# Optimization experiments

Hardware: AMD Instinct MI355X
Metric: run time of the kernel (lower is better)

The kernel has to match this reference:

```python
import jax, jax.numpy as jnp
import numpy as np

EMBED_DIM = 512
NUM_HEADS = 8
HEAD_DIM = EMBED_DIM // NUM_HEADS
B, T, S = 4, 2048, 2048
NEG_INF = jnp.float32(-1e30)


def setup_inputs() -> dict:
    key = jax.random.key(0)
    ks = jax.random.split(key, 12)
    std = 1.0 / np.sqrt(EMBED_DIM)
    d = {
        "query": jax.random.normal(ks[0], (B, T, EMBED_DIM), jnp.float32),
        "key": jax.random.normal(ks[1], (B, S, EMBED_DIM), jnp.float32),
        "value": jax.random.normal(ks[2], (B, S, EMBED_DIM), jnp.float32),
        "key_padding_mask": jnp.zeros((B, S), dtype=bool),
        "attn_mask": jnp.zeros((T, S), dtype=bool),
        "Wq": jax.random.normal(ks[3], (EMBED_DIM, EMBED_DIM), jnp.float32) * std,
        "bq": jnp.zeros((EMBED_DIM,), jnp.float32),
        "Wk": jax.random.normal(ks[4], (EMBED_DIM, EMBED_DIM), jnp.float32) * std,
        "bk": jnp.zeros((EMBED_DIM,), jnp.float32),
        "Wv": jax.random.normal(ks[5], (EMBED_DIM, EMBED_DIM), jnp.float32) * std,
        "bv": jnp.zeros((EMBED_DIM,), jnp.float32),
        "Wo": jax.random.normal(ks[6], (EMBED_DIM, EMBED_DIM), jnp.float32) * std,
        "bo": jnp.zeros((EMBED_DIM,), jnp.float32),
    }
    return d


def reference(query, key, value, key_padding_mask, attn_mask,
              Wq, bq, Wk, bk, Wv, bv, Wo, bo):
    scaling = HEAD_DIM ** (-0.5)
    # projections; Wx stored as [in, out] equivalent of torch Linear weight^T
    q = (query @ Wq + bq) * scaling            # [B, T, E]
    k = key @ Wk + bk                          # [B, S, E]
    v = value @ Wv + bv                        # [B, S, E]
    # split heads -> [B, H, T, Dh]
    q = q.reshape(B, T, NUM_HEADS, HEAD_DIM).transpose(0, 2, 1, 3)
    k = k.reshape(B, S, NUM_HEADS, HEAD_DIM).transpose(0, 2, 1, 3)
    v = v.reshape(B, S, NUM_HEADS, HEAD_DIM).transpose(0, 2, 1, 3)
    scores = jnp.einsum('bhtd,bhsd->bhts', q, k)  # [B, H, T, S]
    scores = jnp.where(attn_mask[None, None, :, :], NEG_INF, scores)
    scores = jnp.where(key_padding_mask[:, None, None, :], NEG_INF, scores)
    attn_weights = jax.nn.softmax(scores, axis=-1)
    # dropout=0 (eval/deterministic): attn_probs == attn_weights
    attn = jnp.einsum('bhts,bhsd->bhtd', attn_weights, v)
    attn = attn.transpose(0, 2, 1, 3).reshape(B, T, EMBED_DIM)
    output = attn @ Wo + bo
    return output, attn_weights
```

## Files before the change

### kernel.cpp

```cpp
#include <hip/hip_runtime.h>
#include <stdint.h>

#define BB 4
#define TT 2048
#define SS 2048
#define EE 512
#define HH 8
#define DH 64
#define NEG_INF_F (-1e30f)

__global__ __launch_bounds__(256) void proj_gemm(const float* __restrict__ A,
        const float* __restrict__ W, const float* __restrict__ bias,
        float* __restrict__ C, float alpha) {
    const int K = EE, N = EE;
    __shared__ float As[16][128 + 4];
    __shared__ float Bs[16][64 + 4];
    const int tid = threadIdx.x;
    const int tx = tid & 15;
    const int ty = tid >> 4;
    const int bm = blockIdx.y * 128;
    const int bn = blockIdx.x * 64;
    float acc[8][4] = {};
    for (int k0 = 0; k0 < K; k0 += 16) {
        #pragma unroll
        for (int j = 0; j < 2; ++j) {
            int f = tid + 256 * j;
            int row = f >> 2;
            int c4 = f & 3;
            float4 v = *reinterpret_cast<const float4*>(
                &A[(size_t)(bm + row) * K + k0 + c4 * 4]);
            As[c4 * 4 + 0][row] = v.x;
            As[c4 * 4 + 1][row] = v.y;
            As[c4 * 4 + 2][row] = v.z;
            As[c4 * 4 + 3][row] = v.w;
        }
        {
            int row = tid >> 4;
            int c4 = tid & 15;
            float4 v = *reinterpret_cast<const float4*>(
                &W[(size_t)(k0 + row) * N + bn + c4 * 4]);
            *reinterpret_cast<float4*>(&Bs[row][c4 * 4]) = v;
        }
        __syncthreads();
        #pragma unroll
        for (int kk = 0; kk < 16; ++kk) {
            float a[8], b[4];
            #pragma unroll
            for (int i = 0; i < 8; ++i) a[i] = As[kk][ty * 8 + i];
            #pragma unroll
            for (int j = 0; j < 4; ++j) b[j] = Bs[kk][tx * 4 + j];
            #pragma unroll
            for (int i = 0; i < 8; ++i)
                #pragma unroll
                for (int j = 0; j < 4; ++j)
                    acc[i][j] = fmaf(a[i], b[j], acc[i][j]);
        }
        __syncthreads();
    }
    #pragma unroll
    for (int i = 0; i < 8; ++i) {
        float4 o;
        o.x = (acc[i][0] + bias[bn + tx * 4 + 0]) * alpha;
        o.y = (acc[i][1] + bias[bn + tx * 4 + 1]) * alpha;
        o.z = (acc[i][2] + bias[bn + tx * 4 + 2]) * alpha;
        o.w = (acc[i][3] + bias[bn + tx * 4 + 3]) * alpha;
        *reinterpret_cast<float4*>(
            &C[(size_t)(bm + ty * 8 + i) * N + bn + tx * 4]) = o;
    }
}

__global__ __launch_bounds__(256) void scores_kernel(const float* __restrict__ q,
        const float* __restrict__ k, const uint8_t* __restrict__ am,
        const uint8_t* __restrict__ kpm, float* __restrict__ Sc) {
    const int bh = blockIdx.z;
    const int b = bh >> 3, h = bh & 7;
    const int t0 = blockIdx.y * 64;
    const int s0 = blockIdx.x * 64;
    __shared__ float Qs[DH][64 + 4];
    __shared__ float Ks[DH][64 + 4];
    const int tid = threadIdx.x;
    #pragma unroll
    for (int j = 0; j < 4; ++j) {
        int f = tid + 256 * j;
        int row = f >> 4;
        int c4 = f & 15;
        float4 vq = *reinterpret_cast<const float4*>(
            &q[(size_t)(b * TT + t0 + row) * EE + h * DH + c4 * 4]);
        Qs[c4 * 4 + 0][row] = vq.x; Qs[c4 * 4 + 1][row] = vq.y;
        Qs[c4 * 4 + 2][row] = vq.z; Qs[c4 * 4 + 3][row] = vq.w;
        float4 vk = *reinterpret_cast<const float4*>(
            &k[(size_t)(b * SS + s0 + row) * EE + h * DH + c4 * 4]);
        Ks[c4 * 4 + 0][row] = vk.x; Ks[c4 * 4 + 1][row] = vk.y;
        Ks[c4 * 4 + 2][row] = vk.z; Ks[c4 * 4 + 3][row] = vk.w;
    }
    __syncthreads();
    const int tx = tid & 15, ty = tid >> 4;
    float acc[4][4] = {};
    #pragma unroll 8
    for (int d = 0; d < DH; ++d) {
        float a[4], bv[4];
        #pragma unroll
        for (int i = 0; i < 4; ++i) a[i] = Qs[d][ty * 4 + i];
        #pragma unroll
        for (int j = 0; j < 4; ++j) bv[j] = Ks[d][tx * 4 + j];
        #pragma unroll
        for (int i = 0; i < 4; ++i)
            #pragma unroll
            for (int j = 0; j < 4; ++j)
                acc[i][j] = fmaf(a[i], bv[j], acc[i][j]);
    }
    uchar4 kv = *reinterpret_cast<const uchar4*>(&kpm[b * SS + s0 + tx * 4]);
    #pragma unroll
    for (int i = 0; i < 4; ++i) {
        int t = t0 + ty * 4 + i;
        uchar4 amv = *reinterpret_cast<const uchar4*>(
            &am[(size_t)t * SS + s0 + tx * 4]);
        float4 o;
        o.x = (amv.x | kv.x) ? NEG_INF_F : acc[i][0];
        o.y = (amv.y | kv.y) ? NEG_INF_F : acc[i][1];
        o.z = (amv.z | kv.z) ? NEG_INF_F : acc[i][2];
        o.w = (amv.w | kv.w) ? NEG_INF_F : acc[i][3];
        *reinterpret_cast<float4*>(
            &Sc[((size_t)bh * TT + t) * SS + s0 + tx * 4]) = o;
    }
}

__device__ __forceinline__ float wred_max(float v) {
    #pragma unroll
    for (int off = 32; off > 0; off >>= 1) v = fmaxf(v, __shfl_xor(v, off));
    return v;
}
__device__ __forceinline__ float wred_sum(float v) {
    #pragma unroll
    for (int off = 32; off > 0; off >>= 1) v += __shfl_xor(v, off);
    return v;
}

__global__ __launch_bounds__(256) void softmax_kernel(float* __restrict__ P) {
    const size_t base = (size_t)blockIdx.x * SS;
    const int tid = threadIdx.x;
    float4 x0 = *reinterpret_cast<const float4*>(&P[base + (size_t)tid * 4]);
    float4 x1 = *reinterpret_cast<const float4*>(&P[base + (size_t)(tid + 256) * 4]);
    float m = fmaxf(fmaxf(fmaxf(x0.x, x0.y), fmaxf(x0.z, x0.w)),
                    fmaxf(fmaxf(x1.x, x1.y), fmaxf(x1.z, x1.w)));
    m = wred_max(m);
    __shared__ float rmax[4];
    __shared__ float rsum[4];
    const int wid = tid >> 6, lane = tid & 63;
    if (lane == 0) rmax[wid] = m;
    __syncthreads();
    m = fmaxf(fmaxf(rmax[0], rmax[1]), fmaxf(rmax[2], rmax[3]));
    x0.x = __expf(x0.x - m); x0.y = __expf(x0.y - m);
    x0.z = __expf(x0.z - m); x0.w = __expf(x0.w - m);
    x1.x = __expf(x1.x - m); x1.y = __expf(x1.y - m);
    x1.z = __expf(x1.z - m); x1.w = __expf(x1.w - m);
    float s = x0.x + x0.y + x0.z + x0.w + x1.x + x1.y + x1.z + x1.w;
    s = wred_sum(s);
    if (lane == 0) rsum[wid] = s;
    __syncthreads();
    s = rsum[0] + rsum[1] + rsum[2] + rsum[3];
    const float inv = 1.0f / s;
    x0.x *= inv; x0.y *= inv; x0.z *= inv; x0.w *= inv;
    x1.x *= inv; x1.y *= inv; x1.z *= inv; x1.w *= inv;
    *reinterpret_cast<float4*>(&P[base + (size_t)tid * 4]) = x0;
    *reinterpret_cast<float4*>(&P[base + (size_t)(tid + 256) * 4]) = x1;
}

__global__ __launch_bounds__(256) void pv_kernel(const float* __restrict__ P,
        const float* __restrict__ v, float* __restrict__ ctx) {
    const int bh = blockIdx.y;
    const int b = bh >> 3, h = bh & 7;
    const int t0 = blockIdx.x * 128;
    __shared__ float Ps[16][128 + 4];
    __shared__ float Vs[16][64 + 4];
    const int tid = threadIdx.x;
    const int tx = tid & 15, ty = tid >> 4;
    float acc[8][4] = {};
    for (int s0 = 0; s0 < SS; s0 += 16) {
        #pragma unroll
        for (int j = 0; j < 2; ++j) {
            int f = tid + 256 * j;
            int row = f >> 2;
            int c4 = f & 3;
            float4 pv = *reinterpret_cast<const float4*>(
                &P[((size_t)bh * TT + t0 + row) * SS + s0 + c4 * 4]);
            Ps[c4 * 4 + 0][row] = pv.x; Ps[c4 * 4 + 1][row] = pv.y;
            Ps[c4 * 4 + 2][row] = pv.z; Ps[c4 * 4 + 3][row] = pv.w;
        }
        {
            int row = tid >> 4, c4 = tid & 15;
            float4 vv = *reinterpret_cast<const float4*>(
                &v[(size_t)(b * SS + s0 + row) * EE + h * DH + c4 * 4]);
            *reinterpret_cast<float4*>(&Vs[row][c4 * 4]) = vv;
        }
        __syncthreads();
        #pragma unroll
        for (int kk = 0; kk < 16; ++kk) {
            float a[8], bv[4];
            #pragma unroll
            for (int i = 0; i < 8; ++i) a[i] = Ps[kk][ty * 8 + i];
            #pragma unroll
            for (int j = 0; j < 4; ++j) bv[j] = Vs[kk][tx * 4 + j];
            #pragma unroll
            for (int i = 0; i < 8; ++i)
                #pragma unroll
                for (int j = 0; j < 4; ++j)
                    acc[i][j] = fmaf(a[i], bv[j], acc[i][j]);
        }
        __syncthreads();
    }
    #pragma unroll
    for (int i = 0; i < 8; ++i) {
        float4 o = make_float4(acc[i][0], acc[i][1], acc[i][2], acc[i][3]);
        *reinterpret_cast<float4*>(
            &ctx[(size_t)(b * TT + t0 + ty * 8 + i) * EE + h * DH + tx * 4]) = o;
    }
}

extern "C" void kernel_launch(void* const* d_in, const int* in_sizes, int n_in,
                              void* d_out, int out_size, void* d_ws, size_t ws_size,
                              hipStream_t stream) {
    const float*   query = (const float*)d_in[0];
    const float*   key   = (const float*)d_in[1];
    const float*   value = (const float*)d_in[2];
    const uint8_t* kpm   = (const uint8_t*)d_in[3];
    const uint8_t* am    = (const uint8_t*)d_in[4];
    const float* Wq = (const float*)d_in[5];  const float* bq = (const float*)d_in[6];
    const float* Wk = (const float*)d_in[7];  const float* bk = (const float*)d_in[8];
    const float* Wv = (const float*)d_in[9];  const float* bv = (const float*)d_in[10];
    const float* Wo = (const float*)d_in[11]; const float* bo = (const float*)d_in[12];

    float* out   = (float*)d_out;
    const size_t BTE = (size_t)BB * TT * EE;
    float* attnW = out + BTE;
    float* ws  = (float*)d_ws;
    float* qp  = ws;
    float* kp  = ws + BTE;
    float* vp  = ws + 2 * BTE;
    float* ctx = qp;

    const float scaling = 0.125f;
    dim3 gProj(EE / 64, (BB * TT) / 128);

    proj_gemm<<<gProj, 256, 0, stream>>>(query, Wq, bq, qp, scaling);
    proj_gemm<<<gProj, 256, 0, stream>>>(key,   Wk, bk, kp, 1.0f);
    proj_gemm<<<gProj, 256, 0, stream>>>(value, Wv, bv, vp, 1.0f);

    scores_kernel<<<dim3(SS / 64, TT / 64, BB * HH), 256, 0, stream>>>(
        qp, kp, am, kpm, attnW);
    softmax_kernel<<<BB * HH * TT, 256, 0, stream>>>(attnW);
    pv_kernel<<<dim3(TT / 128, BB * HH), 256, 0, stream>>>(attnW, vp, ctx);

    proj_gemm<<<gProj, 256, 0, stream>>>(ctx, Wo, bo, out, 1.0f);
}
```

Before: 1.451 ms.

## Fuse scores and softmax with two-pass bf16 MFMA, MFMA PV with transposed V

Replaces the separate scores, softmax and PV kernels with a two-pass kernel. The first pass computes QK^T using bf16 MFMA and keeps running max and sum, and the second recomputes scores and writes normalized probabilities. This removes the full write-then-read-modify-write of the attention-weight matrix. PV now uses bf16 MFMA, with V written transposed by a dedicated projection kernel. The cost is recomputing QK^T, reduced precision from bf16 inputs, and scattered scalar stores of attention weights and mask bytes, which may be poorly coalesced.

Result: faster. 1.298 ms (-10.5%).

```diff
diff --git a/kernel.cpp b/kernel.cpp
--- a/kernel.cpp
+++ b/kernel.cpp
@@ -9,6 +9,37 @@
 #define DH 64
 #define NEG_INF_F (-1e30f)
 
+using short8 = __attribute__((ext_vector_type(8))) short;
+using f32x4  = __attribute__((ext_vector_type(4))) float;
+
+__device__ __forceinline__ unsigned short f2bf(float f) {
+    unsigned int u = __float_as_uint(f);
+    unsigned int r = (u + 0x7FFFu + ((u >> 16) & 1u)) >> 16;
+    return (unsigned short)r;
+}
+__device__ __forceinline__ unsigned int pack2(float a, float b) {
+    return (unsigned int)f2bf(a) | ((unsigned int)f2bf(b) << 16);
+}
+__device__ __forceinline__ short8 cvt_frag(float4 a, float4 b) {
+    short8 r;
+    r[0] = (short)f2bf(a.x); r[1] = (short)f2bf(a.y);
+    r[2] = (short)f2bf(a.z); r[3] = (short)f2bf(a.w);
+    r[4] = (short)f2bf(b.x); r[5] = (short)f2bf(b.y);
+    r[6] = (short)f2bf(b.z); r[7] = (short)f2bf(b.w);
+    return r;
+}
+
+__device__ __forceinline__ void stage_tile_bf16(const float* src_base, size_t row_stride,
+        unsigned short (*dst)[72], int tid) {
+    const int row = tid >> 2;
+    const int cg  = (tid & 3) * 16;
+    const float4* s4 = reinterpret_cast<const float4*>(src_base + (size_t)row * row_stride + cg);
+    float4 a = s4[0], b = s4[1], c = s4[2], d = s4[3];
+    uint4* d4 = reinterpret_cast<uint4*>(&dst[row][cg]);
+    d4[0] = make_uint4(pack2(a.x, a.y), pack2(a.z, a.w), pack2(b.x, b.y), pack2(b.z, b.w));
+    d4[1] = make_uint4(pack2(c.x, c.y), pack2(c.z, c.w), pack2(d.x, d.y), pack2(d.z, d.w));
+}
+
 __global__ __launch_bounds__(256) void proj_gemm(const float* __restrict__ A,
         const float* __restrict__ W, const float* __restrict__ bias,
         float* __restrict__ C, float alpha) {
@@ -16,29 +47,21 @@
     __shared__ float As[16][128 + 4];
     __shared__ float Bs[16][64 + 4];
     const int tid = threadIdx.x;
-    const int tx = tid & 15;
-    const int ty = tid >> 4;
-    const int bm = blockIdx.y * 128;
-    const int bn = blockIdx.x * 64;
+    const int tx = tid & 15, ty = tid >> 4;
+    const int bm = blockIdx.y * 128, bn = blockIdx.x * 64;
     float acc[8][4] = {};
     for (int k0 = 0; k0 < K; k0 += 16) {
         #pragma unroll
         for (int j = 0; j < 2; ++j) {
             int f = tid + 256 * j;
-            int row = f >> 2;
-            int c4 = f & 3;
-            float4 v = *reinterpret_cast<const float4*>(
-                &A[(size_t)(bm + row) * K + k0 + c4 * 4]);
-            As[c4 * 4 + 0][row] = v.x;
-            As[c4 * 4 + 1][row] = v.y;
-            As[c4 * 4 + 2][row] = v.z;
-            As[c4 * 4 + 3][row] = v.w;
+            int row = f >> 2, c4 = f & 3;
+            float4 v = *reinterpret_cast<const float4*>(&A[(size_t)(bm + row) * K + k0 + c4 * 4]);
+            As[c4 * 4 + 0][row] = v.x; As[c4 * 4 + 1][row] = v.y;
+            As[c4 * 4 + 2][row] = v.z; As[c4 * 4 + 3][row] = v.w;
         }
         {
-            int row = tid >> 4;
-            int c4 = tid & 15;
-            float4 v = *reinterpret_cast<const float4*>(
-                &W[(size_t)(k0 + row) * N + bn + c4 * 4]);
+            int row = tid >> 4, c4 = tid & 15;
+            float4 v = *reinterpret_cast<const float4*>(&W[(size_t)(k0 + row) * N + bn + c4 * 4]);
             *reinterpret_cast<float4*>(&Bs[row][c4 * 4]) = v;
         }
         __syncthreads();
@@ -64,157 +87,214 @@
         o.y = (acc[i][1] + bias[bn + tx * 4 + 1]) * alpha;
         o.z = (acc[i][2] + bias[bn + tx * 4 + 2]) * alpha;
         o.w = (acc[i][3] + bias[bn + tx * 4 + 3]) * alpha;
-        *reinterpret_cast<float4*>(
-            &C[(size_t)(bm + ty * 8 + i) * N + bn + tx * 4]) = o;
-    }
-}
-
-__global__ __launch_bounds__(256) void scores_kernel(const float* __restrict__ q,
-        const float* __restrict__ k, const uint8_t* __restrict__ am,
-        const uint8_t* __restrict__ kpm, float* __restrict__ Sc) {
-    const int bh = blockIdx.z;
-    const int b = bh >> 3, h = bh & 7;
-    const int t0 = blockIdx.y * 64;
-    const int s0 = blockIdx.x * 64;
-    __shared__ float Qs[DH][64 + 4];
-    __shared__ float Ks[DH][64 + 4];
-    const int tid = threadIdx.x;
-    #pragma unroll
-    for (int j = 0; j < 4; ++j) {
-        int f = tid + 256 * j;
-        int row = f >> 4;
-        int c4 = f & 15;
-        float4 vq = *reinterpret_cast<const float4*>(
-            &q[(size_t)(b * TT + t0 + row) * EE + h * DH + c4 * 4]);
-        Qs[c4 * 4 + 0][row] = vq.x; Qs[c4 * 4 + 1][row] = vq.y;
-        Qs[c4 * 4 + 2][row] = vq.z; Qs[c4 * 4 + 3][row] = vq.w;
-        float4 vk = *reinterpret_cast<const float4*>(
-            &k[(size_t)(b * SS + s0 + row) * EE + h * DH + c4 * 4]);
-        Ks[c4 * 4 + 0][row] = vk.x; Ks[c4 * 4 + 1][row] = vk.y;
-        Ks[c4 * 4 + 2][row] = vk.z; Ks[c4 * 4 + 3][row] = vk.w;
-    }
-    __syncthreads();
-    const int tx = tid & 15, ty = tid >> 4;
-    float acc[4][4] = {};
-    #pragma unroll 8
-    for (int d = 0; d < DH; ++d) {
-        float a[4], bv[4];
-        #pragma unroll
-        for (int i = 0; i < 4; ++i) a[i] = Qs[d][ty * 4 + i];
-        #pragma unroll
-        for (int j = 0; j < 4; ++j) bv[j] = Ks[d][tx * 4 + j];
-        #pragma unroll
-        for (int i = 0; i < 4; ++i)
-            #pragma unroll
-            for (int j = 0; j < 4; ++j)
-                acc[i][j] = fmaf(a[i], bv[j], acc[i][j]);
-    }
-    uchar4 kv = *reinterpret_cast<const uchar4*>(&kpm[b * SS + s0 + tx * 4]);
-    #pragma unroll
-    for (int i = 0; i < 4; ++i) {
-        int t = t0 + ty * 4 + i;
-        uchar4 amv = *reinterpret_cast<const uchar4*>(
-            &am[(size_t)t * SS + s0 + tx * 4]);
-        float4 o;
-        o.x = (amv.x | kv.x) ? NEG_INF_F : acc[i][0];
-        o.y = (amv.y | kv.y) ? NEG_INF_F : acc[i][1];
-        o.z = (amv.z | kv.z) ? NEG_INF_F : acc[i][2];
-        o.w = (amv.w | kv.w) ? NEG_INF_F : acc[i][3];
-        *reinterpret_cast<float4*>(
-            &Sc[((size_t)bh * TT + t) * SS + s0 + tx * 4]) = o;
-    }
-}
-
-__device__ __forceinline__ float wred_max(float v) {
-    #pragma unroll
-    for (int off = 32; off > 0; off >>= 1) v = fmaxf(v, __shfl_xor(v, off));
-    return v;
-}
-__device__ __forceinline__ float wred_sum(float v) {
-    #pragma unroll
-    for (int off = 32; off > 0; off >>= 1) v += __shfl_xor(v, off);
-    return v;
-}
-
-__global__ __launch_bounds__(256) void softmax_kernel(float* __restrict__ P) {
-    const size_t base = (size_t)blockIdx.x * SS;
-    const int tid = threadIdx.x;
-    float4 x0 = *reinterpret_cast<const float4*>(&P[base + (size_t)tid * 4]);
-    float4 x1 = *reinterpret_cast<const float4*>(&P[base + (size_t)(tid + 256) * 4]);
-    float m = fmaxf(fmaxf(fmaxf(x0.x, x0.y), fmaxf(x0.z, x0.w)),
-                    fmaxf(fmaxf(x1.x, x1.y), fmaxf(x1.z, x1.w)));
-    m = wred_max(m);
-    __shared__ float rmax[4];
-    __shared__ float rsum[4];
-    const int wid = tid >> 6, lane = tid & 63;
-    if (lane == 0) rmax[wid] = m;
-    __syncthreads();
-    m = fmaxf(fmaxf(rmax[0], rmax[1]), fmaxf(rmax[2], rmax[3]));
-    x0.x = __expf(x0.x - m); x0.y = __expf(x0.y - m);
-    x0.z = __expf(x0.z - m); x0.w = __expf(x0.w - m);
-    x1.x = __expf(x1.x - m); x1.y = __expf(x1.y - m);
-    x1.z = __expf(x1.z - m); x1.w = __expf(x1.w - m);
-    float s = x0.x + x0.y + x0.z + x0.w + x1.x + x1.y + x1.z + x1.w;
-    s = wred_sum(s);
-    if (lane == 0) rsum[wid] = s;
-    __syncthreads();
-    s = rsum[0] + rsum[1] + rsum[2] + rsum[3];
-    const float inv = 1.0f / s;
-    x0.x *= inv; x0.y *= inv; x0.z *= inv; x0.w *= inv;
-    x1.x *= inv; x1.y *= inv; x1.z *= inv; x1.w *= inv;
-    *reinterpret_cast<float4*>(&P[base + (size_t)tid * 4]) = x0;
-    *reinterpret_cast<float4*>(&P[base + (size_t)(tid + 256) * 4]) = x1;
-}
-
-__global__ __launch_bounds__(256) void pv_kernel(const float* __restrict__ P,
-        const float* __restrict__ v, float* __restrict__ ctx) {
-    const int bh = blockIdx.y;
-    const int b = bh >> 3, h = bh & 7;
-    const int t0 = blockIdx.x * 128;
-    __shared__ float Ps[16][128 + 4];
-    __shared__ float Vs[16][64 + 4];
+        *reinterpret_cast<float4*>(&C[(size_t)(bm + ty * 8 + i) * N + bn + tx * 4]) = o;
+    }
+}
+
+__global__ __launch_bounds__(256) void proj_gemm_vT(const float* __restrict__ A,
+        const float* __restrict__ W, const float* __restrict__ bias,
+        float* __restrict__ vpT) {
+    const int K = EE, N = EE;
+    __shared__ float As[16][128 + 4];
+    __shared__ float Bs[16][64 + 4];
     const int tid = threadIdx.x;
     const int tx = tid & 15, ty = tid >> 4;
+    const int bm = blockIdx.y * 128, bn = blockIdx.x * 64;
     float acc[8][4] = {};
-    for (int s0 = 0; s0 < SS; s0 += 16) {
+    for (int k0 = 0; k0 < K; k0 += 16) {
         #pragma unroll
         for (int j = 0; j < 2; ++j) {
             int f = tid + 256 * j;
-            int row = f >> 2;
-            int c4 = f & 3;
-            float4 pv = *reinterpret_cast<const float4*>(
-                &P[((size_t)bh * TT + t0 + row) * SS + s0 + c4 * 4]);
-            Ps[c4 * 4 + 0][row] = pv.x; Ps[c4 * 4 + 1][row] = pv.y;
-            Ps[c4 * 4 + 2][row] = pv.z; Ps[c4 * 4 + 3][row] = pv.w;
+            int row = f >> 2, c4 = f & 3;
+            float4 v = *reinterpret_cast<const float4*>(&A[(size_t)(bm + row) * K + k0 + c4 * 4]);
+            As[c4 * 4 + 0][row] = v.x; As[c4 * 4 + 1][row] = v.y;
+            As[c4 * 4 + 2][row] = v.z; As[c4 * 4 + 3][row] = v.w;
         }
         {
             int row = tid >> 4, c4 = tid & 15;
-            float4 vv = *reinterpret_cast<const float4*>(
-                &v[(size_t)(b * SS + s0 + row) * EE + h * DH + c4 * 4]);
-            *reinterpret_cast<float4*>(&Vs[row][c4 * 4]) = vv;
+            float4 v = *reinterpret_cast<const float4*>(&W[(size_t)(k0 + row) * N + bn + c4 * 4]);
+            *reinterpret_cast<float4*>(&Bs[row][c4 * 4]) = v;
         }
         __syncthreads();
         #pragma unroll
         for (int kk = 0; kk < 16; ++kk) {
-            float a[8], bv[4];
-            #pragma unroll
-            for (int i = 0; i < 8; ++i) a[i] = Ps[kk][ty * 8 + i];
-            #pragma unroll
-            for (int j = 0; j < 4; ++j) bv[j] = Vs[kk][tx * 4 + j];
+            float a[8], b[4];
+            #pragma unroll
+            for (int i = 0; i < 8; ++i) a[i] = As[kk][ty * 8 + i];
+            #pragma unroll
+            for (int j = 0; j < 4; ++j) b[j] = Bs[kk][tx * 4 + j];
             #pragma unroll
             for (int i = 0; i < 8; ++i)
                 #pragma unroll
                 for (int j = 0; j < 4; ++j)
-                    acc[i][j] = fmaf(a[i], bv[j], acc[i][j]);
-        }
-        __syncthreads();
-    }
-    #pragma unroll
-    for (int i = 0; i < 8; ++i) {
-        float4 o = make_float4(acc[i][0], acc[i][1], acc[i][2], acc[i][3]);
-        *reinterpret_cast<float4*>(
-            &ctx[(size_t)(b * TT + t0 + ty * 8 + i) * EE + h * DH + tx * 4]) = o;
-    }
+                    acc[i][j] = fmaf(a[i], b[j], acc[i][j]);
+        }
+        __syncthreads();
+    }
+    const int bb = bm >> 11;
+    const int sb = (bm & (SS - 1)) + ty * 8;
+    #pragma unroll
+    for (int j = 0; j < 4; ++j) {
+        const int n = bn + tx * 4 + j;
+        const float bvj = bias[n];
+        float4 o0 = make_float4(acc[0][j] + bvj, acc[1][j] + bvj, acc[2][j] + bvj, acc[3][j] + bvj);
+        float4 o1 = make_float4(acc[4][j] + bvj, acc[5][j] + bvj, acc[6][j] + bvj, acc[7][j] + bvj);
+        float* dst = &vpT[((size_t)bb * EE + n) * SS + sb];
+        *reinterpret_cast<float4*>(dst) = o0;
+        *reinterpret_cast<float4*>(dst + 4) = o1;
+    }
+}
+
+__global__ __launch_bounds__(256) void flash_scores(const float* __restrict__ qp,
+        const float* __restrict__ kp, const uint8_t* __restrict__ am,
+        const uint8_t* __restrict__ kpm, float* __restrict__ attnW) {
+    const int bh = blockIdx.y;
+    const int b = bh >> 3, h = bh & 7;
+    const int t0 = blockIdx.x * 64;
+    __shared__ unsigned short Ks[64][72];
+    const int tid = threadIdx.x;
+    const int lane = tid & 63, wid = tid >> 6;
+    const int lc = lane & 15, lg = lane >> 4;
+
+    short8 aq[2];
+    {
+        const float* qrow = &qp[(size_t)(b * TT + t0 + wid * 16 + lc) * EE + h * DH];
+        #pragma unroll
+        for (int kc = 0; kc < 2; ++kc) {
+            float4 f0 = *reinterpret_cast<const float4*>(qrow + kc * 32 + lg * 8);
+            float4 f1 = *reinterpret_cast<const float4*>(qrow + kc * 32 + lg * 8 + 4);
+            aq[kc] = cvt_frag(f0, f1);
+        }
+    }
+    const int trow = t0 + wid * 16 + lg * 4;
+    float mrun[4], lrun[4];
+    #pragma unroll
+    for (int r = 0; r < 4; ++r) { mrun[r] = -3.0e38f; lrun[r] = 0.0f; }
+
+    for (int st = 0; st < 32; ++st) {
+        const int s0 = st * 64;
+        stage_tile_bf16(&kp[(size_t)(b * SS + s0) * EE + h * DH], EE, Ks, tid);
+        __syncthreads();
+        float sv[4][4];
+        float tmax[4];
+        #pragma unroll
+        for (int r = 0; r < 4; ++r) tmax[r] = -3.0e38f;
+        #pragma unroll
+        for (int ct = 0; ct < 4; ++ct) {
+            const int brow = ct * 16 + lc;
+            short8 b0 = *reinterpret_cast<const short8*>(&Ks[brow][lg * 8]);
+            short8 b1 = *reinterpret_cast<const short8*>(&Ks[brow][32 + lg * 8]);
+            f32x4 c = {0.0f, 0.0f, 0.0f, 0.0f};
+            c = __builtin_amdgcn_mfma_f32_16x16x32_bf16(aq[0], b0, c, 0, 0, 0);
+            c = __builtin_amdgcn_mfma_f32_16x16x32_bf16(aq[1], b1, c, 0, 0, 0);
+            const int s = s0 + ct * 16 + lc;
+            const bool kpb = kpm[b * SS + s] != 0;
+            #pragma unroll
+            for (int r = 0; r < 4; ++r) {
+                const bool mk = kpb || (am[(size_t)(trow + r) * SS + s] != 0);
+                const float scv = mk ? NEG_INF_F : c[r];
+                sv[ct][r] = scv;
+                tmax[r] = fmaxf(tmax[r], scv);
+            }
+        }
+        __syncthreads();
+        #pragma unroll
+        for (int r = 0; r < 4; ++r) {
+            #pragma unroll
+            for (int mm = 8; mm >= 1; mm >>= 1)
+                tmax[r] = fmaxf(tmax[r], __shfl_xor(tmax[r], mm, 16));
+        }
+        float ts[4] = {0.0f, 0.0f, 0.0f, 0.0f};
+        #pragma unroll
+        for (int ct = 0; ct < 4; ++ct)
+            #pragma unroll
+            for (int r = 0; r < 4; ++r) {
+                const float mnew = fmaxf(mrun[r], tmax[r]);
+                ts[r] += __expf(sv[ct][r] - mnew);
+            }
+        #pragma unroll
+        for (int r = 0; r < 4; ++r) {
+            const float mnew = fmaxf(mrun[r], tmax[r]);
+            #pragma unroll
+            for (int mm = 8; mm >= 1; mm >>= 1)
+                ts[r] += __shfl_xor(ts[r], mm, 16);
+            lrun[r] = lrun[r] * __expf(mrun[r] - mnew) + ts[r];
+            mrun[r] = mnew;
+        }
+    }
+    float linv[4];
+    #pragma unroll
+    for (int r = 0; r < 4; ++r) linv[r] = 1.0f / lrun[r];
+
+    for (int st = 0; st < 32; ++st) {
+        const int s0 = st * 64;
+        stage_tile_bf16(&kp[(size_t)(b * SS + s0) * EE + h * DH], EE, Ks, tid);
+        __syncthreads();
+        #pragma unroll
+        for (int ct = 0; ct < 4; ++ct) {
+            const int brow = ct * 16 + lc;
+            short8 b0 = *reinterpret_cast<const short8*>(&Ks[brow][lg * 8]);
+            short8 b1 = *reinterpret_cast<const short8*>(&Ks[brow][32 + lg * 8]);
+            f32x4 c = {0.0f, 0.0f, 0.0f, 0.0f};
+            c = __builtin_amdgcn_mfma_f32_16x16x32_bf16(aq[0], b0, c, 0, 0, 0);
+            c = __builtin_amdgcn_mfma_f32_16x16x32_bf16(aq[1], b1, c, 0, 0, 0);
+            const int s = s0 + ct * 16 + lc;
+            const bool kpb = kpm[b * SS + s] != 0;
+            #pragma unroll
+            for (int r = 0; r < 4; ++r) {
+                const bool mk = kpb || (am[(size_t)(trow + r) * SS + s] != 0);
+                const float scv = mk ? NEG_INF_F : c[r];
+                const float p = __expf(scv - mrun[r]) * linv[r];
+                attnW[((size_t)bh * TT + trow + r) * SS + s] = p;
+            }
+        }
+        __syncthreads();
+    }
+}
+
+__global__ __launch_bounds__(256) void pv_mfma(const float* __restrict__ P,
+        const float* __restrict__ vpT, float* __restrict__ ctx) {
+    const int bh = blockIdx.y;
+    const int b = bh >> 3, h = bh & 7;
+    const int t0 = blockIdx.x * 64;
+    __shared__ unsigned short Vt[64][72];
+    const int tid = threadIdx.x;
+    const int lane = tid & 63, wid = tid >> 6;
+    const int lc = lane & 15, lg = lane >> 4;
+
+    f32x4 acc[4];
+    #pragma unroll
+    for (int ct = 0; ct < 4; ++ct) acc[ct] = (f32x4){0.0f, 0.0f, 0.0f, 0.0f};
+
+    const float* prow = &P[((size_t)bh * TT + t0 + wid * 16 + lc) * SS];
+
+    for (int st = 0; st < 32; ++st) {
+        const int s0 = st * 64;
+        stage_tile_bf16(&vpT[((size_t)b * EE + h * DH) * SS + s0], SS, Vt, tid);
+        __syncthreads();
+        short8 ap[2];
+        #pragma unroll
+        for (int kc = 0; kc < 2; ++kc) {
+            float4 f0 = *reinterpret_cast<const float4*>(prow + s0 + kc * 32 + lg * 8);
+            float4 f1 = *reinterpret_cast<const float4*>(prow + s0 + kc * 32 + lg * 8 + 4);
+            ap[kc] = cvt_frag(f0, f1);
+        }
+        #pragma unroll
+        for (int ct = 0; ct < 4; ++ct) {
+            const int brow = ct * 16 + lc;
+            short8 b0 = *reinterpret_cast<const short8*>(&Vt[brow][lg * 8]);
+            short8 b1 = *reinterpret_cast<const short8*>(&Vt[brow][32 + lg * 8]);
+            acc[ct] = __builtin_amdgcn_mfma_f32_16x16x32_bf16(ap[0], b0, acc[ct], 0, 0, 0);
+            acc[ct] = __builtin_amdgcn_mfma_f32_16x16x32_bf16(ap[1], b1, acc[ct], 0, 0, 0);
+        }
+        __syncthreads();
+    }
+    const int trow = t0 + wid * 16 + lg * 4;
+    #pragma unroll
+    for (int ct = 0; ct < 4; ++ct)
+        #pragma unroll
+        for (int r = 0; r < 4; ++r)
+            ctx[(size_t)(b * TT + trow + r) * EE + h * DH + ct * 16 + lc] = acc[ct][r];
 }
 
 extern "C" void kernel_launch(void* const* d_in, const int* in_sizes, int n_in,
@@ -236,20 +316,18 @@
     float* ws  = (float*)d_ws;
     float* qp  = ws;
     float* kp  = ws + BTE;
-    float* vp  = ws + 2 * BTE;
+    float* vpT = ws + 2 * BTE;
     float* ctx = qp;
 
     const float scaling = 0.125f;
     dim3 gProj(EE / 64, (BB * TT) / 128);
 
-    proj_gemm<<<gProj, 256, 0, stream>>>(query, Wq, bq, qp, scaling);
-    proj_gemm<<<gProj, 256, 0, stream>>>(key,   Wk, bk, kp, 1.0f);
-    proj_gemm<<<gProj, 256, 0, stream>>>(value, Wv, bv, vp, 1.0f);
-
-    scores_kernel<<<dim3(SS / 64, TT / 64, BB * HH), 256, 0, stream>>>(
-        qp, kp, am, kpm, attnW);
-    softmax_kernel<<<BB * HH * TT, 256, 0, stream>>>(attnW);
-    pv_kernel<<<dim3(TT / 128, BB * HH), 256, 0, stream>>>(attnW, vp, ctx);
-
-    proj_gemm<<<gProj, 256, 0, stream>>>(ctx, Wo, bo, out, 1.0f);
-}
+    proj_gemm   <<<gProj, 256, 0, stream>>>(query, Wq, bq, qp, scaling);
+    proj_gemm   <<<gProj, 256, 0, stream>>>(key,   Wk, bk, kp, 1.0f);
+    proj_gemm_vT<<<gProj, 256, 0, stream>>>(value, Wv, bv, vpT);
+
+    flash_scores<<<dim3(TT / 64, BB * HH), 256, 0, stream>>>(qp, kp, am, kpm, attnW);
+    pv_mfma     <<<dim3(TT / 64, BB * HH), 256, 0, stream>>>(attnW, vpT, ctx);
+
+    proj_gemm   <<<gProj, 256, 0, stream>>>(ctx, Wo, bo, out, 1.0f);
+}
```
